# Kernel tuning notes

Hardware: AMD Instinct MI355X
Metric: run time of the kernel (lower is better)

Reference implementation:

```python
import jax, jax.numpy as jnp
import numpy as np

B, T, C, H = 2, 2048, 1024, 16
D = C // H  # head_dim = 64


def setup_inputs() -> dict:
    key = jax.random.key(0)
    ks = jax.random.split(key, 12)
    s = 1.0 / np.sqrt(C)
    inp = {
        "q": jax.random.normal(ks[0], (B, T, C), jnp.float32),
        "k": jax.random.normal(ks[1], (B, T, C), jnp.float32),
        "v": jax.random.normal(ks[2], (B, T, C), jnp.float32),
        "mask": jnp.tril(jnp.ones((T, T), jnp.int32)),  # causal mask; 0 = masked
        "Wq": jax.random.normal(ks[3], (C, C), jnp.float32) * s,
        "bq": jax.random.normal(ks[4], (C,), jnp.float32) * s,
        "Wk": jax.random.normal(ks[5], (C, C), jnp.float32) * s,
        "bk": jax.random.normal(ks[6], (C,), jnp.float32) * s,
        "Wv": jax.random.normal(ks[7], (C, C), jnp.float32) * s,
        "bv": jax.random.normal(ks[8], (C,), jnp.float32) * s,
        "Wo": jax.random.normal(ks[9], (C, C), jnp.float32) * s,
        "bo": jax.random.normal(ks[10], (C,), jnp.float32) * s,
    }
    return inp


def reference(q, k, v, mask, Wq, bq, Wk, bk, Wv, bv, Wo, bo):
    # Linear projections (torch Linear: x @ W.T + b)
    qh = (q @ Wq.T + bq).reshape(B, T, H, D).transpose(0, 2, 1, 3)  # [B,H,T,D]
    kh = (k @ Wk.T + bk).reshape(B, -1, H, D).transpose(0, 2, 1, 3)
    vh = (v @ Wv.T + bv).reshape(B, -1, H, D).transpose(0, 2, 1, 3)
    scores = jnp.einsum("bhtd,bhsd->bhts", qh, kh) / jnp.sqrt(jnp.float32(D))
    scores = jnp.where(mask[None, None, :, :] == 0, -jnp.inf, scores)
    attn = jax.nn.softmax(scores, axis=-1)
    out = jnp.einsum("bhts,bhsd->bhtd", attn, vh)  # [B,H,T,D]
    out = out.transpose(0, 2, 1, 3).reshape(B, T, C)
    return out @ Wo.T + bo
```

## Files before the change

kernel.cpp:

```cpp
#include <hip/hip_runtime.h>
#include <hip/hip_bf16.h>

#define BB 2
#define TT 2048
#define CC 1024
#define HH 16
#define DD 64
#define MM (BB * TT)

typedef __bf16 bf16;
typedef __bf16 bf16x4 __attribute__((ext_vector_type(4)));
typedef __bf16 bf16x8 __attribute__((ext_vector_type(8)));
typedef float f32x4 __attribute__((ext_vector_type(4)));

__device__ __forceinline__ void gload16(const bf16* g, bf16* l) {
    __builtin_amdgcn_global_load_lds(
        (__attribute__((address_space(1))) void*)g,
        (__attribute__((address_space(3))) void*)l, 16, 0, 0);
}

__global__ __launch_bounds__(256) void to_bf16(
    const float* __restrict__ q, const float* __restrict__ k,
    const float* __restrict__ v,
    const float* __restrict__ wq, const float* __restrict__ wk,
    const float* __restrict__ wv, const float* __restrict__ wo,
    bf16* __restrict__ xq, bf16* __restrict__ xk, bf16* __restrict__ xv,
    bf16* __restrict__ owq, bf16* __restrict__ owk, bf16* __restrict__ owv,
    bf16* __restrict__ owo)
{
    const unsigned XE = 1u << 22;
    const unsigned WE = 1u << 20;
    const unsigned NC = (3u * XE + 4u * WE) >> 3;
    for (unsigned c = blockIdx.x * blockDim.x + threadIdx.x; c < NC;
         c += gridDim.x * blockDim.x) {
        const unsigned e = c << 3;
        const float* src; bf16* dst; unsigned off;
        if (e < 3u * XE) {
            const unsigned t = e >> 22; off = e & (XE - 1u);
            src = (t == 0) ? q : (t == 1) ? k : v;
            dst = (t == 0) ? xq : (t == 1) ? xk : xv;
        } else {
            const unsigned e2 = e - 3u * XE;
            const unsigned t = e2 >> 20; off = e2 & (WE - 1u);
            src = (t == 0) ? wq : (t == 1) ? wk : (t == 2) ? wv : wo;
            dst = (t == 0) ? owq : (t == 1) ? owk : (t == 2) ? owv : owo;
        }
        const f32x4 a = *reinterpret_cast<const f32x4*>(src + off);
        const f32x4 b = *reinterpret_cast<const f32x4*>(src + off + 4);
        bf16x8 r;
#pragma unroll
        for (int j = 0; j < 4; ++j) { r[j] = (bf16)a[j]; r[j + 4] = (bf16)b[j]; }
        *reinterpret_cast<bf16x8*>(dst + off) = r;
    }
}

template <typename TOUT, int HEAD_LAYOUT>
__device__ __forceinline__ void gemm_tile_body(
    const bf16* __restrict__ X, const bf16* __restrict__ W,
    const float* __restrict__ bias, TOUT* __restrict__ out,
    bf16* lA, bf16* lB, int vmode, int bx, int by)
{
    const int tid  = threadIdx.x;
    const int lane = tid & 63;
    const int quad = lane >> 4;
    const int lm   = lane & 15;
    const int wave = tid >> 6;
    const int m0 = bx << 7;
    const int n0 = by << 7;
    const int wrow = (wave >> 1) << 6;
    const int wcol = (wave & 1) << 6;

    const int c0 = tid, c1 = tid + 256;
    const bf16* gA0 = X + (size_t)(m0 + (c0 >> 2)) * CC + (c0 & 3) * 8;
    const bf16* gA1 = X + (size_t)(m0 + (c1 >> 2)) * CC + (c1 & 3) * 8;
    const bf16* gB0 = W + (size_t)(n0 + (c0 >> 2)) * CC + (c0 & 3) * 8;
    const bf16* gB1 = W + (size_t)(n0 + (c1 >> 2)) * CC + (c1 & 3) * 8;
    bf16* lAw0 = lA + wave * 512;
    bf16* lAw1 = lA + 2048 + wave * 512;
    bf16* lBw0 = lB + wave * 512;
    bf16* lBw1 = lB + 2048 + wave * 512;

    f32x4 acc[4][4];
#pragma unroll
    for (int i = 0; i < 4; ++i)
#pragma unroll
        for (int j = 0; j < 4; ++j) acc[i][j] = (f32x4){0.f, 0.f, 0.f, 0.f};

    for (int kk = 0; kk < CC; kk += 32) {
        __syncthreads();
        gload16(gA0 + kk, lAw0);
        gload16(gA1 + kk, lAw1);
        gload16(gB0 + kk, lBw0);
        gload16(gB1 + kk, lBw1);
        __syncthreads();

        bf16x8 af[4], bf_[4];
#pragma unroll
        for (int i = 0; i < 4; ++i)
            af[i] = *reinterpret_cast<const bf16x8*>(
                lA + (wrow + i * 16 + lm) * 32 + quad * 8);
#pragma unroll
        for (int j = 0; j < 4; ++j)
            bf_[j] = *reinterpret_cast<const bf16x8*>(
                lB + (wcol + j * 16 + lm) * 32 + quad * 8);
#pragma unroll
        for (int i = 0; i < 4; ++i)
#pragma unroll
            for (int j = 0; j < 4; ++j)
                acc[i][j] = __builtin_amdgcn_mfma_f32_16x16x32_bf16(
                    af[i], bf_[j], acc[i][j], 0, 0, 0);
    }

#pragma unroll
    for (int j = 0; j < 4; ++j) {
        const int col = n0 + wcol + j * 16 + lm;
        const float bv = bias[col];
        if (vmode) {
            const int h = col / DD, d = col % DD;
#pragma unroll
            for (int i = 0; i < 4; ++i) {
                const int m = m0 + wrow + i * 16 + quad * 4;
                const int b_ = m / TT, t = m % TT;
                bf16x4 o;
#pragma unroll
                for (int r = 0; r < 4; ++r) o[r] = (bf16)(acc[i][j][r] + bv);
                *reinterpret_cast<bf16x4*>(
                    (bf16*)out + (((size_t)(b_ * HH + h)) * DD + d) * TT + t) = o;
            }
        } else {
#pragma unroll
            for (int i = 0; i < 4; ++i)
#pragma unroll
                for (int r = 0; r < 4; ++r) {
                    const int m = m0 + wrow + i * 16 + quad * 4 + r;
                    const float v = acc[i][j][r] + bv;
                    if (HEAD_LAYOUT) {
                        const int b_ = m / TT, t = m % TT;
                        const int h = col / DD, d = col % DD;
                        out[(((size_t)(b_ * HH + h)) * TT + t) * DD + d] = (TOUT)v;
                    } else {
                        out[(size_t)m * CC + col] = (TOUT)v;
                    }
                }
        }
    }
}

__global__ __launch_bounds__(256) void gemm_qkv(
    const bf16* __restrict__ x0, const bf16* __restrict__ x1,
    const bf16* __restrict__ x2,
    const bf16* __restrict__ w0, const bf16* __restrict__ w1,
    const bf16* __restrict__ w2,
    const float* __restrict__ b0, const float* __restrict__ b1,
    const float* __restrict__ b2,
    bf16* __restrict__ o0, bf16* __restrict__ o1, bf16* __restrict__ o2)
{
    __shared__ __align__(16) bf16 lA[128 * 32];
    __shared__ __align__(16) bf16 lB[128 * 32];
    const int flat = blockIdx.x + 32 * blockIdx.y + 256 * blockIdx.z;
    const int swz  = (flat & 7) * 96 + (flat >> 3);
    const int by   = swz & 7;
    const int t    = swz >> 3;
    const int bx   = t & 31;
    const int z    = t >> 5;
    const bf16* X = (z == 0) ? x0 : (z == 1) ? x1 : x2;
    const bf16* W = (z == 0) ? w0 : (z == 1) ? w1 : w2;
    const float* bias = (z == 0) ? b0 : (z == 1) ? b1 : b2;
    bf16* out = (z == 0) ? o0 : (z == 1) ? o1 : o2;
    gemm_tile_body<bf16, 1>(X, W, bias, out, lA, lB, (z == 2) ? 1 : 0, bx, by);
}

__global__ __launch_bounds__(256) void gemm_oproj(
    const bf16* __restrict__ X, const bf16* __restrict__ W,
    const float* __restrict__ bias, float* __restrict__ out)
{
    __shared__ __align__(16) bf16 lA[64 * 32];
    __shared__ __align__(16) bf16 lB[128 * 32];
    const int tid  = threadIdx.x;
    const int lane = tid & 63;
    const int quad = lane >> 4;
    const int lm   = lane & 15;
    const int wave = tid >> 6;
    const int flat = blockIdx.x + 64 * blockIdx.y;
    const int swz  = (flat & 7) * 64 + (flat >> 3);
    const int by   = swz & 7;
    const int bx   = swz >> 3;
    const int m0 = bx << 6;
    const int n0 = by << 7;
    const int wrow = (wave >> 1) << 5;
    const int wcol = (wave & 1) << 6;

    const int cA = tid;
    const int c0 = tid, c1 = tid + 256;
    const bf16* gA0 = X + (size_t)(m0 + (cA >> 2)) * CC + (cA & 3) * 8;
    const bf16* gB0 = W + (size_t)(n0 + (c0 >> 2)) * CC + (c0 & 3) * 8;
    const bf16* gB1 = W + (size_t)(n0 + (c1 >> 2)) * CC + (c1 & 3) * 8;
    bf16* lAw  = lA + wave * 512;
    bf16* lBw0 = lB + wave * 512;
    bf16* lBw1 = lB + 2048 + wave * 512;

    f32x4 acc[2][4];
#pragma unroll
    for (int i = 0; i < 2; ++i)
#pragma unroll
        for (int j = 0; j < 4; ++j) acc[i][j] = (f32x4){0.f, 0.f, 0.f, 0.f};

    for (int kk = 0; kk < CC; kk += 32) {
        __syncthreads();
        gload16(gA0 + kk, lAw);
        gload16(gB0 + kk, lBw0);
        gload16(gB1 + kk, lBw1);
        __syncthreads();

        bf16x8 af[2], bf_[4];
#pragma unroll
        for (int i = 0; i < 2; ++i)
            af[i] = *reinterpret_cast<const bf16x8*>(
                lA + (wrow + i * 16 + lm) * 32 + quad * 8);
#pragma unroll
        for (int j = 0; j < 4; ++j)
            bf_[j] = *reinterpret_cast<const bf16x8*>(
                lB + (wcol + j * 16 + lm) * 32 + quad * 8);
#pragma unroll
        for (int i = 0; i < 2; ++i)
#pragma unroll
            for (int j = 0; j < 4; ++j)
                acc[i][j] = __builtin_amdgcn_mfma_f32_16x16x32_bf16(
                    af[i], bf_[j], acc[i][j], 0, 0, 0);
    }

#pragma unroll
    for (int j = 0; j < 4; ++j) {
        const int col = n0 + wcol + j * 16 + lm;
        const float bv = bias[col];
#pragma unroll
        for (int i = 0; i < 2; ++i)
#pragma unroll
            for (int r = 0; r < 4; ++r) {
                const int m = m0 + wrow + i * 16 + quad * 4 + r;
                out[(size_t)m * CC + col] = acc[i][j][r] + bv;
            }
    }
}

__device__ __forceinline__ void issue_k(const bf16* __restrict__ Kh,
                                        size_t baseQK, int s0, int kKey,
                                        int kDc, bf16x8* kreg) {
#pragma unroll
    for (int it = 0; it < 2; ++it)
        kreg[it] = *reinterpret_cast<const bf16x8*>(
            Kh + baseQK + (size_t)(s0 + kKey + it * 32) * DD + kDc * 8);
}
__device__ __forceinline__ void issue_v(const bf16* __restrict__ Vt,
                                        size_t baseVT, int s0, int vD,
                                        int vSc, bf16x8* vreg) {
#pragma unroll
    for (int it = 0; it < 2; ++it)
        vreg[it] = *reinterpret_cast<const bf16x8*>(
            Vt + baseVT + (size_t)vD * TT + s0 + (vSc + it * 4) * 8);
}
__device__ __forceinline__ void write_k(bf16* buf, int kKey, int kDc,
                                        const bf16x8* kreg) {
#pragma unroll
    for (int it = 0; it < 2; ++it)
        *reinterpret_cast<bf16x8*>(&buf[(kKey + it * 32) * 72 + kDc * 8]) =
            kreg[it];
}
__device__ __forceinline__ void write_v(bf16* buf, int vD, int vSc,
                                        const bf16x8* vreg) {
#pragma unroll
    for (int it = 0; it < 2; ++it) {
        const int sc = vSc + it * 4;
        const int c2 = sc >> 2, h = (sc >> 1) & 1, q0 = (sc & 1) * 2;
        bf16x4 lo, hi;
#pragma unroll
        for (int j = 0; j < 4; ++j) { lo[j] = vreg[it][j]; hi[j] = vreg[it][4 + j]; }
        *reinterpret_cast<bf16x4*>(
            &buf[((c2 * 4 + q0) * 64 + vD) * 8 + h * 4]) = lo;
        *reinterpret_cast<bf16x4*>(
            &buf[((c2 * 4 + q0 + 1) * 64 + vD) * 8 + h * 4]) = hi;
    }
}
__device__ __forceinline__ void qk_tile(const bf16* bufK, int lm, int koff,
                                        bf16x8 qf0, bf16x8 qf1,
                                        float sv[4][4]) {
#pragma unroll
    for (int st = 0; st < 4; ++st) {
        const bf16* kp = &bufK[(st * 16 + lm) * 72 + koff];
        bf16x8 k0 = *reinterpret_cast<const bf16x8*>(kp);
        bf16x8 k1 = *reinterpret_cast<const bf16x8*>(kp + 32);
        f32x4 s = {0.f, 0.f, 0.f, 0.f};
        s = __builtin_amdgcn_mfma_f32_16x16x32_bf16(k0, qf0, s, 0, 0, 0);
        s = __builtin_amdgcn_mfma_f32_16x16x32_bf16(k1, qf1, s, 0, 0, 0);
#pragma unroll
        for (int r = 0; r < 4; ++r) sv[st][r] = s[r];
    }
}

#define SM_SHIFT 12.0f

__global__ __launch_bounds__(256) void attn_fused(
    const bf16* __restrict__ Qh, const bf16* __restrict__ Kh,
    const bf16* __restrict__ Vt, bf16* __restrict__ attn_out)
{
    __shared__ __align__(16) bf16 ldsK[4][64 * 72];
    __shared__ __align__(16) bf16 ldsV[4][8 * 64 * 8];

    const int tid  = threadIdx.x;
    const int lane = tid & 63;
    const int wave = tid >> 6;
    const int flat = blockIdx.x + 16 * blockIdx.y;
    const int swz  = (flat & 7) * 64 + (flat >> 3);
    const int xp = swz & 15;
    const int bh = swz >> 4;
    const int b_ = bh >> 4, h = bh & 15;
    const size_t baseQK = (size_t)bh * TT * DD;
    const size_t baseVT = (size_t)bh * DD * TT;
    const int lm   = lane & 15;
    const int quad = lane >> 4;
    const int koff = quad * 8;

    const int kKey = tid >> 3, kDc = tid & 7;
    const int vD   = tid >> 2, vSc = tid & 3;

    for (int pass = 0; pass < 2; ++pass) {
        const int qb = pass == 0 ? (TT / 64 - 1 - xp) : xp;
        const int q0 = qb * 64 + wave * 16;
        const int q_lane = q0 + lm;
        const int ntiles = qb + 1;
        const int npairs = ntiles >> 1;
        const int has_tail = ntiles & 1;

        const bf16* qp = Qh + baseQK + (size_t)q_lane * DD + koff;
        bf16x8 qr0 = *reinterpret_cast<const bf16x8*>(qp);
        bf16x8 qr1 = *reinterpret_cast<const bf16x8*>(qp + 32);
        bf16x8 qf0, qf1;
#pragma unroll
        for (int j = 0; j < 8; ++j) {
            qf0[j] = (bf16)((float)qr0[j] * 0.125f);
            qf1[j] = (bf16)((float)qr1[j] * 0.125f);
        }

        f32x4 Oacc[4];
#pragma unroll
        for (int dt = 0; dt < 4; ++dt) Oacc[dt] = (f32x4){0.f, 0.f, 0.f, 0.f};
        float l_run = 0.f;

        bf16x8 kregA[2], vregA[2], kregB[2], vregB[2];
        issue_k(Kh, baseQK, 0, kKey, kDc, kregA);
        issue_v(Vt, baseVT, 0, vD, vSc, vregA);
        if (ntiles > 1) {
            issue_k(Kh, baseQK, 64, kKey, kDc, kregB);
            issue_v(Vt, baseVT, 64, vD, vSc, vregB);
        }
        __syncthreads();

        int base = 0;
        for (int j = 0; j < npairs; ++j) {
            const int t1 = 2 * j + 1;

            write_k(ldsK[base], kKey, kDc, kregA);
            write_v(ldsV[base], vD, vSc, vregA);
            write_k(ldsK[base + 1], kKey, kDc, kregB);
            write_v(ldsV[base + 1], vD, vSc, vregB);
            __syncthreads();

            if (t1 + 1 < ntiles) {
                issue_k(Kh, baseQK, (t1 + 1) * 64, kKey, kDc, kregA);
                issue_v(Vt, baseVT, (t1 + 1) * 64, vD, vSc, vregA);
            }
            if (t1 + 2 < ntiles) {
                issue_k(Kh, baseQK, (t1 + 2) * 64, kKey, kDc, kregB);
                issue_v(Vt, baseVT, (t1 + 2) * 64, vD, vSc, vregB);
            }

            float svA[4][4], svB[4][4];
            __builtin_amdgcn_s_setprio(1);
            qk_tile(ldsK[base], lm, koff, qf0, qf1, svA);
            qk_tile(ldsK[base + 1], lm, koff, qf0, qf1, svB);
            __builtin_amdgcn_s_setprio(0);

            if (t1 == qb) {
                const int s0b = t1 * 64;
#pragma unroll
                for (int st = 0; st < 4; ++st) {
                    const int kbase = s0b + st * 16 + quad * 4;
#pragma unroll
                    for (int r = 0; r < 4; ++r)
                        if (kbase + r > q_lane) svB[st][r] = -1e30f;
                }
            }

            float ps[8];
#pragma unroll
            for (int st = 0; st < 4; ++st) {
                float p0 = __expf(svA[st][0] - SM_SHIFT);
                float p1 = __expf(svA[st][1] - SM_SHIFT);
                float p2 = __expf(svA[st][2] - SM_SHIFT);
                float p3 = __expf(svA[st][3] - SM_SHIFT);
                svA[st][0] = p0; svA[st][1] = p1; svA[st][2] = p2; svA[st][3] = p3;
                ps[st] = (p0 + p1) + (p2 + p3);
                float b0 = __expf(svB[st][0] - SM_SHIFT);
                float b1 = __expf(svB[st][1] - SM_SHIFT);
                float b2 = __expf(svB[st][2] - SM_SHIFT);
                float b3 = __expf(svB[st][3] - SM_SHIFT);
                svB[st][0] = b0; svB[st][1] = b1; svB[st][2] = b2; svB[st][3] = b3;
                ps[4 + st] = (b0 + b1) + (b2 + b3);
            }
            float srow = ((ps[0] + ps[1]) + (ps[2] + ps[3]))
                       + ((ps[4] + ps[5]) + (ps[6] + ps[7]));
            srow += __shfl_xor(srow, 16);
            srow += __shfl_xor(srow, 32);
            l_run += srow;

            bf16x8 pf[4];
#pragma unroll
            for (int c = 0; c < 2; ++c)
#pragma unroll
                for (int jj = 0; jj < 4; ++jj) {
                    pf[c][jj]         = (bf16)svA[2 * c][jj];
                    pf[c][4 + jj]     = (bf16)svA[2 * c + 1][jj];
                    pf[2 + c][jj]     = (bf16)svB[2 * c][jj];
                    pf[2 + c][4 + jj] = (bf16)svB[2 * c + 1][jj];
                }

            __builtin_amdgcn_s_setprio(1);
#pragma unroll
            for (int dt = 0; dt < 4; ++dt) {
                const int d = dt * 16 + lm;
#pragma unroll
                for (int c = 0; c < 4; ++c) {
                    const bf16* vp = &ldsV[base + (c >> 1)]
                        [(((c & 1) * 4 + quad) * 64 + d) * 8];
                    bf16x8 vf = *reinterpret_cast<const bf16x8*>(vp);
                    Oacc[dt] = __builtin_amdgcn_mfma_f32_16x16x32_bf16(
                        vf, pf[c], Oacc[dt], 0, 0, 0);
                }
            }
            __builtin_amdgcn_s_setprio(0);
            base ^= 2;
        }

        if (has_tail) {
            write_k(ldsK[base], kKey, kDc, kregA);
            write_v(ldsV[base], vD, vSc, vregA);
            __syncthreads();

            float sv[4][4];
            __builtin_amdgcn_s_setprio(1);
            qk_tile(ldsK[base], lm, koff, qf0, qf1, sv);
            __builtin_amdgcn_s_setprio(0);
            const int s0 = qb * 64;
#pragma unroll
            for (int st = 0; st < 4; ++st) {
                const int kbase = s0 + st * 16 + quad * 4;
#pragma unroll
                for (int r = 0; r < 4; ++r)
                    if (kbase + r > q_lane) sv[st][r] = -1e30f;
            }
            float ps[4];
#pragma unroll
            for (int st = 0; st < 4; ++st) {
                float p0 = __expf(sv[st][0] - SM_SHIFT);
                float p1 = __expf(sv[st][1] - SM_SHIFT);
                float p2 = __expf(sv[st][2] - SM_SHIFT);
                float p3 = __expf(sv[st][3] - SM_SHIFT);
                sv[st][0] = p0; sv[st][1] = p1; sv[st][2] = p2; sv[st][3] = p3;
                ps[st] = (p0 + p1) + (p2 + p3);
            }
            float srow = (ps[0] + ps[1]) + (ps[2] + ps[3]);
            srow += __shfl_xor(srow, 16);
            srow += __shfl_xor(srow, 32);
            l_run += srow;

            bf16x8 pf[2];
#pragma unroll
            for (int c = 0; c < 2; ++c)
#pragma unroll
                for (int jj = 0; jj < 4; ++jj) {
                    pf[c][jj]     = (bf16)sv[2 * c][jj];
                    pf[c][4 + jj] = (bf16)sv[2 * c + 1][jj];
                }
            __builtin_amdgcn_s_setprio(1);
#pragma unroll
            for (int dt = 0; dt < 4; ++dt) {
                const int d = dt * 16 + lm;
#pragma unroll
                for (int c = 0; c < 2; ++c) {
                    const bf16* vp = &ldsV[base][((c * 4 + quad) * 64 + d) * 8];
                    bf16x8 vf = *reinterpret_cast<const bf16x8*>(vp);
                    Oacc[dt] = __builtin_amdgcn_mfma_f32_16x16x32_bf16(
                        vf, pf[c], Oacc[dt], 0, 0, 0);
                }
            }
            __builtin_amdgcn_s_setprio(0);
        }

        const float inv_l = 1.0f / l_run;
        bf16* dst = attn_out + ((size_t)(b_ * TT + q_lane)) * CC + h * DD;
#pragma unroll
        for (int dt = 0; dt < 4; ++dt) {
            bf16x4 o;
#pragma unroll
            for (int r = 0; r < 4; ++r) o[r] = (bf16)(Oacc[dt][r] * inv_l);
            *reinterpret_cast<bf16x4*>(dst + dt * 16 + quad * 4) = o;
        }
    }
}

extern "C" void kernel_launch(void* const* d_in, const int* in_sizes, int n_in,
                              void* d_out, int out_size, void* d_ws,
                              size_t ws_size, hipStream_t stream)
{
    const float* q  = (const float*)d_in[0];
    const float* k  = (const float*)d_in[1];
    const float* v  = (const float*)d_in[2];
    const float* Wq = (const float*)d_in[4];
    const float* bq = (const float*)d_in[5];
    const float* Wk = (const float*)d_in[6];
    const float* bk = (const float*)d_in[7];
    const float* Wv = (const float*)d_in[8];
    const float* bv = (const float*)d_in[9];
    const float* Wo = (const float*)d_in[10];
    const float* bo = (const float*)d_in[11];
    float* out = (float*)d_out;

    bf16* Qh   = (bf16*)d_ws;
    bf16* Kh   = Qh + (size_t)MM * CC;
    bf16* Vt   = Kh + (size_t)MM * CC;
    bf16* attn = Vt + (size_t)MM * CC;
    bf16* Xq   = attn + (size_t)MM * CC;
    bf16* Xk   = Xq + (size_t)MM * CC;
    bf16* Xv   = Xk + (size_t)MM * CC;
    bf16* Wqb  = Xv + (size_t)MM * CC;
    bf16* Wkb  = Wqb + (size_t)CC * CC;
    bf16* Wvb  = Wkb + (size_t)CC * CC;
    bf16* Wob  = Wvb + (size_t)CC * CC;

    const dim3 blk(256);
    to_bf16<<<dim3(2048), blk, 0, stream>>>(
        q, k, v, Wq, Wk, Wv, Wo, Xq, Xk, Xv, Wqb, Wkb, Wvb, Wob);
    gemm_qkv<<<dim3(32, 8, 3), blk, 0, stream>>>(
        Xq, Xk, Xv, Wqb, Wkb, Wvb, bq, bk, bv, Qh, Kh, Vt);
    attn_fused<<<dim3(TT / 128, BB * HH), blk, 0, stream>>>(Qh, Kh, Vt, attn);
    gemm_oproj<<<dim3(64, 8), blk, 0, stream>>>(
        attn, Wob, bo, out);
}
```

Measured before the change: 215.0 us.

## Double-buffer QKV GEMM LDS tiles with register prefetch of next K slice

Replaces the direct global-to-LDS loads and the two barriers per K step in the QKV projection GEMM with a register-staged, double-buffered pipeline. The next K slice is loaded into registers while MFMAs run on the current LDS buffer, then written to the alternate buffer, leaving one barrier per iteration. This aims to hide global load latency behind compute, at the cost of doubled LDS usage (32 KB per block) and extra VGPRs, which may reduce occupancy.

Result: no change. 218.1 us (+1.4%).

```diff
diff --git a/kernel.cpp b/kernel.cpp
--- a/kernel.cpp
+++ b/kernel.cpp
@@ -64,9 +64,9 @@
     const int lane = tid & 63;
     const int quad = lane >> 4;
     const int lm   = lane & 15;
-    const int wave = tid >> 6;
     const int m0 = bx << 7;
     const int n0 = by << 7;
+    const int wave = tid >> 6;
     const int wrow = (wave >> 1) << 6;
     const int wcol = (wave & 1) << 6;
 
@@ -75,10 +75,6 @@
     const bf16* gA1 = X + (size_t)(m0 + (c1 >> 2)) * CC + (c1 & 3) * 8;
     const bf16* gB0 = W + (size_t)(n0 + (c0 >> 2)) * CC + (c0 & 3) * 8;
     const bf16* gB1 = W + (size_t)(n0 + (c1 >> 2)) * CC + (c1 & 3) * 8;
-    bf16* lAw0 = lA + wave * 512;
-    bf16* lAw1 = lA + 2048 + wave * 512;
-    bf16* lBw0 = lB + wave * 512;
-    bf16* lBw1 = lB + 2048 + wave * 512;
 
     f32x4 acc[4][4];
 #pragma unroll
@@ -86,29 +82,44 @@
 #pragma unroll
         for (int j = 0; j < 4; ++j) acc[i][j] = (f32x4){0.f, 0.f, 0.f, 0.f};
 
+    bf16x8 ra0 = *reinterpret_cast<const bf16x8*>(gA0);
+    bf16x8 ra1 = *reinterpret_cast<const bf16x8*>(gA1);
+    bf16x8 rb0 = *reinterpret_cast<const bf16x8*>(gB0);
+    bf16x8 rb1 = *reinterpret_cast<const bf16x8*>(gB1);
+
+    int cur = 0;
     for (int kk = 0; kk < CC; kk += 32) {
+        bf16* la = lA + cur * 4096;
+        bf16* lb = lB + cur * 4096;
+        *reinterpret_cast<bf16x8*>(la + c0 * 8) = ra0;
+        *reinterpret_cast<bf16x8*>(la + c1 * 8) = ra1;
+        *reinterpret_cast<bf16x8*>(lb + c0 * 8) = rb0;
+        *reinterpret_cast<bf16x8*>(lb + c1 * 8) = rb1;
         __syncthreads();
-        gload16(gA0 + kk, lAw0);
-        gload16(gA1 + kk, lAw1);
-        gload16(gB0 + kk, lBw0);
-        gload16(gB1 + kk, lBw1);
-        __syncthreads();
+
+        if (kk + 32 < CC) {
+            ra0 = *reinterpret_cast<const bf16x8*>(gA0 + kk + 32);
+            ra1 = *reinterpret_cast<const bf16x8*>(gA1 + kk + 32);
+            rb0 = *reinterpret_cast<const bf16x8*>(gB0 + kk + 32);
+            rb1 = *reinterpret_cast<const bf16x8*>(gB1 + kk + 32);
+        }
 
         bf16x8 af[4], bf_[4];
 #pragma unroll
         for (int i = 0; i < 4; ++i)
             af[i] = *reinterpret_cast<const bf16x8*>(
-                lA + (wrow + i * 16 + lm) * 32 + quad * 8);
+                la + (wrow + i * 16 + lm) * 32 + quad * 8);
 #pragma unroll
         for (int j = 0; j < 4; ++j)
             bf_[j] = *reinterpret_cast<const bf16x8*>(
-                lB + (wcol + j * 16 + lm) * 32 + quad * 8);
+                lb + (wcol + j * 16 + lm) * 32 + quad * 8);
 #pragma unroll
         for (int i = 0; i < 4; ++i)
 #pragma unroll
             for (int j = 0; j < 4; ++j)
                 acc[i][j] = __builtin_amdgcn_mfma_f32_16x16x32_bf16(
                     af[i], bf_[j], acc[i][j], 0, 0, 0);
+        cur ^= 1;
     }
 
 #pragma unroll
@@ -155,8 +166,8 @@
     const float* __restrict__ b2,
     bf16* __restrict__ o0, bf16* __restrict__ o1, bf16* __restrict__ o2)
 {
-    __shared__ __align__(16) bf16 lA[128 * 32];
-    __shared__ __align__(16) bf16 lB[128 * 32];
+    __shared__ __align__(16) bf16 lA[2 * 128 * 32];
+    __shared__ __align__(16) bf16 lB[2 * 128 * 32];
     const int flat = blockIdx.x + 32 * blockIdx.y + 256 * blockIdx.z;
     const int swz  = (flat & 7) * 96 + (flat >> 3);
     const int by   = swz & 7;
```
